# Performance work log

Measured on AMD Instinct MI355X. Metric: run time of the kernel, lower is better.

The kernel has to match this reference:

```python
import jax, jax.numpy as jnp
import numpy as np
from jax import lax

T, B, IN, H, OUT = 2048, 128, 2, 200, 1


def setup_inputs() -> dict:
    key = jax.random.key(0)
    ks = jax.random.split(key, 7)
    s_ih = 1.0 / np.sqrt(H)
    return {
        "input_seq": jax.random.normal(ks[0], (T, B, IN), dtype=jnp.float32),
        "W_ih": jax.random.normal(ks[1], (H, IN), dtype=jnp.float32) * s_ih,
        "W_hh": jax.random.normal(ks[2], (H, H), dtype=jnp.float32) * s_ih,
        "b_ih": jax.random.normal(ks[3], (H,), dtype=jnp.float32) * s_ih,
        "b_hh": jax.random.normal(ks[4], (H,), dtype=jnp.float32) * s_ih,
        "W_out": jax.random.normal(ks[5], (OUT, H), dtype=jnp.float32) * s_ih,
        "b_out": jax.random.normal(ks[6], (OUT,), dtype=jnp.float32) * s_ih,
    }


def reference(input_seq, W_ih, W_hh, b_ih, b_hh, W_out, b_out):
    # torch.nn.RNN (tanh, 1 layer, seq-first): h_t = tanh(x_t W_ih^T + b_ih + h_{t-1} W_hh^T + b_hh)
    # Precompute the input projection for all timesteps (vectorized), fold both biases.
    x_proj = jnp.einsum('tbi,hi->tbh', input_seq, W_ih) + (b_ih + b_hh)  # [T,B,H]

    def step(h, xt):
        h_new = jnp.tanh(xt + h @ W_hh.T)
        return h_new, h_new

    h0 = jnp.zeros((input_seq.shape[1], W_hh.shape[0]), dtype=input_seq.dtype)
    _, hs = lax.scan(step, h0, x_proj)  # hs: [T,B,H]
    # Final linear head applied to every timestep output
    return jnp.einsum('tbh,oh->tbo', hs, W_out) + b_out  # [T,B,1]
```

## Files before the change

kernel.cpp:

```cpp
#include <hip/hip_runtime.h>
#include <hip/hip_fp16.h>


typedef short s8v __attribute__((ext_vector_type(8)));
typedef float f4v __attribute__((ext_vector_type(4)));

static constexpr int T = 2048;
static constexpr int B = 128;
static constexpr int H = 200;
static constexpr int NTHR = 1024;
static constexpr int NT  = 13;
static constexpr int KT  = 7;
static constexpr int HP  = 224;
static constexpr int RS  = 9;

__device__ __forceinline__ unsigned short f2h(float f) {
    const __half h = __float2half_rn(f);
    return *(const unsigned short*)&h;
}
__device__ __forceinline__ float h2f(unsigned short u) {
    const __half h = *(const __half*)&u;
    return __half2float(h);
}

__global__ __attribute__((amdgpu_flat_work_group_size(NTHR, NTHR),
                          amdgpu_waves_per_eu(4, 4)))
void rnn_fused(const float* __restrict__ x,
               const float* __restrict__ W_ih,
               const float* __restrict__ W_hh,
               const float* __restrict__ b_ih,
               const float* __restrict__ b_hh,
               const float* __restrict__ W_out,
               const float* __restrict__ b_out,
               float* __restrict__ out)
{
    const int b    = blockIdx.x;
    const int tid  = threadIdx.x;
    const int w    = tid >> 6;
    const int lane = tid & 63;
    const int m    = lane & 15;
    const int q    = lane >> 4;

    const bool hasT = (w < NT);
    const int  nA   = 16 * w + m;
    const bool colv = hasT && (nA < H);

    __shared__ __align__(16) unsigned short ring[RS][2][HP];
    __shared__ float xs[2 * T];

    for (int i = tid; i < RS * 2 * HP; i += NTHR) (&ring[0][0][0])[i] = 0;
    for (int idx = tid; idx < T; idx += NTHR) {
        const float2 v = *(const float2*)(x + (size_t)idx * (B * 2) + 2 * b);
        xs[2 * idx] = v.x; xs[2 * idx + 1] = v.y;
    }

    s8v BA[KT];
#pragma unroll
    for (int kt = 0; kt < KT; ++kt) {
        s8v ba{};
        if (colv) {
#pragma unroll
            for (int j = 0; j < 8; ++j) {
                const int ks = 32 * kt + 8 * q + j;
                ba[j] = (short)((ks < H) ? f2h(W_hh[nA * H + ks])
                                         : (unsigned short)0);
            }
        }
        BA[kt] = ba;
    }

    const float wxA0 = colv ? W_ih[nA * 2]     : 0.f;
    const float wxA1 = colv ? W_ih[nA * 2 + 1] : 0.f;
    const float bA   = colv ? (b_ih[nA] + b_hh[nA]) : 0.f;

    const float wo0 = W_out[lane];
    const float wo1 = W_out[64 + lane];
    const float wo2 = W_out[128 + lane];
    const float wo3 = (192 + lane < H) ? W_out[192 + lane] : 0.f;
    const float bo  = b_out[0];

    __syncthreads();

    float* op = out + b;

    auto drain = [&](int slot, int tout) {
        float v = (h2f(ring[slot][0][lane])     + h2f(ring[slot][1][lane]))     * wo0
                + (h2f(ring[slot][0][64+lane])  + h2f(ring[slot][1][64+lane]))  * wo1
                + (h2f(ring[slot][0][128+lane]) + h2f(ring[slot][1][128+lane])) * wo2;
        if (lane < 32)
            v += (h2f(ring[slot][0][192+lane]) + h2f(ring[slot][1][192+lane])) * wo3;
#pragma unroll
        for (int off = 32; off > 0; off >>= 1)
            v += __shfl_down(v, off, 64);
        if (lane == 0) op[(size_t)tout * B] = v + bo;
    };

    int rp = 0;
    for (int t = 0; t < T; ++t) {
        if (rp == 0 && t) {
            if (w < RS) drain(w, t - RS + w);
            __syncthreads();
        }
        const int sr = rp ? rp - 1 : RS - 1;
        const int sw = rp;
        const float x0 = xs[2 * t], x1 = xs[2 * t + 1];

        if (hasT) {
            const unsigned short* lp = &ring[sr][(m == 1) ? 1 : 0][8 * q];
            s8v A[KT];
#pragma unroll
            for (int kt = 0; kt < KT; ++kt) A[kt] = *(const s8v*)(lp + 32 * kt);

            f4v u = {0.f, 0.f, 0.f, 0.f};
            f4v v = {0.f, 0.f, 0.f, 0.f};
            u = __builtin_amdgcn_mfma_f32_16x16x32_f16(A[0], BA[0], u, 0, 0, 0);
            v = __builtin_amdgcn_mfma_f32_16x16x32_f16(A[4], BA[4], v, 0, 0, 0);
            u = __builtin_amdgcn_mfma_f32_16x16x32_f16(A[1], BA[1], u, 0, 0, 0);
            v = __builtin_amdgcn_mfma_f32_16x16x32_f16(A[5], BA[5], v, 0, 0, 0);
            u = __builtin_amdgcn_mfma_f32_16x16x32_f16(A[2], BA[2], u, 0, 0, 0);
            v = __builtin_amdgcn_mfma_f32_16x16x32_f16(A[6], BA[6], v, 0, 0, 0);
            u = __builtin_amdgcn_mfma_f32_16x16x32_f16(A[3], BA[3], u, 0, 0, 0);

            if (q == 0 && nA < H) {
                const float y   = (u[0] + u[1]) + (v[0] + v[1]);
                const float pre = y + fmaf(x0, wxA0, fmaf(x1, wxA1, bA));
                const float e   = __expf(2.f * pre);
                const float th  = 1.f - 2.f / (e + 1.f);
                const unsigned short hi = f2h(th);
                ring[sw][0][nA] = hi;
                ring[sw][1][nA] = f2h(th - h2f(hi));
            }
        }
        __syncthreads();
        if (++rp == RS) rp = 0;
    }

    const int rem = T % RS;
    if (w < rem) drain(w, T - rem + w);
}

extern "C" void kernel_launch(void* const* d_in, const int* in_sizes, int n_in,
                              void* d_out, int out_size, void* d_ws, size_t ws_size,
                              hipStream_t stream) {
    const float* x     = (const float*)d_in[0];
    const float* W_ih  = (const float*)d_in[1];
    const float* W_hh  = (const float*)d_in[2];
    const float* b_ih  = (const float*)d_in[3];
    const float* b_hh  = (const float*)d_in[4];
    const float* W_out = (const float*)d_in[5];
    const float* b_out = (const float*)d_in[6];
    float* out = (float*)d_out;

    rnn_fused<<<B, NTHR, 0, stream>>>(x, W_ih, W_hh, b_ih, b_hh, W_out, b_out, out);
}
```

Baseline: 1.114 ms.

## Halve block to 8 waves, each computing two hidden-column tiles per step

Moves the block from 16 waves to 8 and reassigns the 13 hidden-column tiles so most waves compute two tiles, sharing the A fragments loaded from shared memory. The ring buffer shrinks to 8 slots so each wave drains one slot, and the tail drain is simplified because T is divisible by 8. The aim is to make the per-timestep barrier cheaper across fewer waves and to reuse LDS reads, at the cost of longer per-wave MFMA chains and more registers holding the weights.

```diff
diff --git a/kernel.cpp b/kernel.cpp
--- a/kernel.cpp
+++ b/kernel.cpp
@@ -8,11 +8,10 @@
 static constexpr int T = 2048;
 static constexpr int B = 128;
 static constexpr int H = 200;
-static constexpr int NTHR = 1024;
-static constexpr int NT  = 13;
+static constexpr int NTHR = 512;
 static constexpr int KT  = 7;
 static constexpr int HP  = 224;
-static constexpr int RS  = 9;
+static constexpr int RS  = 8;
 
 __device__ __forceinline__ unsigned short f2h(float f) {
     const __half h = __float2half_rn(f);
@@ -24,7 +23,7 @@
 }
 
 __global__ __attribute__((amdgpu_flat_work_group_size(NTHR, NTHR),
-                          amdgpu_waves_per_eu(4, 4)))
+                          amdgpu_waves_per_eu(2, 2)))
 void rnn_fused(const float* __restrict__ x,
                const float* __restrict__ W_ih,
                const float* __restrict__ W_hh,
@@ -41,9 +40,13 @@
     const int m    = lane & 15;
     const int q    = lane >> 4;
 
-    const bool hasT = (w < NT);
-    const int  nA   = 16 * w + m;
-    const bool colv = hasT && (nA < H);
+    const int dfc = (w > 3) + (w > 5) + (w > 6);
+    const int t0  = 2 * w - dfc;
+    const int tn  = (w == 3 || w == 5 || w == 6) ? 1 : 2;
+    const int nA0 = 16 * t0 + m;
+    const int nA1 = 16 * (t0 + 1) + m;
+    const bool cv0 = (nA0 < H);
+    const bool cv1 = (tn > 1) && (nA1 < H);
 
     __shared__ __align__(16) unsigned short ring[RS][2][HP];
     __shared__ float xs[2 * T];
@@ -54,24 +57,35 @@
         xs[2 * idx] = v.x; xs[2 * idx + 1] = v.y;
     }
 
-    s8v BA[KT];
+    s8v BA0[KT], BA1[KT];
 #pragma unroll
     for (int kt = 0; kt < KT; ++kt) {
-        s8v ba{};
-        if (colv) {
+        s8v b0{}, b1{};
+        if (cv0) {
 #pragma unroll
             for (int j = 0; j < 8; ++j) {
                 const int ks = 32 * kt + 8 * q + j;
-                ba[j] = (short)((ks < H) ? f2h(W_hh[nA * H + ks])
+                b0[j] = (short)((ks < H) ? f2h(W_hh[nA0 * H + ks])
                                          : (unsigned short)0);
             }
         }
-        BA[kt] = ba;
+        if (cv1) {
+#pragma unroll
+            for (int j = 0; j < 8; ++j) {
+                const int ks = 32 * kt + 8 * q + j;
+                b1[j] = (short)((ks < H) ? f2h(W_hh[nA1 * H + ks])
+                                         : (unsigned short)0);
+            }
+        }
+        BA0[kt] = b0; BA1[kt] = b1;
     }
 
-    const float wxA0 = colv ? W_ih[nA * 2]     : 0.f;
-    const float wxA1 = colv ? W_ih[nA * 2 + 1] : 0.f;
-    const float bA   = colv ? (b_ih[nA] + b_hh[nA]) : 0.f;
+    const float wx00 = cv0 ? W_ih[nA0 * 2]     : 0.f;
+    const float wx01 = cv0 ? W_ih[nA0 * 2 + 1] : 0.f;
+    const float bA0  = cv0 ? (b_ih[nA0] + b_hh[nA0]) : 0.f;
+    const float wx10 = cv1 ? W_ih[nA1 * 2]     : 0.f;
+    const float wx11 = cv1 ? W_ih[nA1 * 2 + 1] : 0.f;
+    const float bA1  = cv1 ? (b_ih[nA1] + b_hh[nA1]) : 0.f;
 
     const float wo0 = W_out[lane];
     const float wo1 = W_out[64 + lane];
@@ -98,45 +112,84 @@
     int rp = 0;
     for (int t = 0; t < T; ++t) {
         if (rp == 0 && t) {
-            if (w < RS) drain(w, t - RS + w);
+            drain(w, t - RS + w);
             __syncthreads();
         }
         const int sr = rp ? rp - 1 : RS - 1;
         const int sw = rp;
         const float x0 = xs[2 * t], x1 = xs[2 * t + 1];
 
-        if (hasT) {
-            const unsigned short* lp = &ring[sr][(m == 1) ? 1 : 0][8 * q];
-            s8v A[KT];
-#pragma unroll
-            for (int kt = 0; kt < KT; ++kt) A[kt] = *(const s8v*)(lp + 32 * kt);
-
+        const unsigned short* lp = &ring[sr][(m == 1) ? 1 : 0][8 * q];
+        s8v A[KT];
+#pragma unroll
+        for (int kt = 0; kt < KT; ++kt) A[kt] = *(const s8v*)(lp + 32 * kt);
+
+        if (tn == 2) {
+            f4v u0 = {0.f, 0.f, 0.f, 0.f};
+            f4v v0 = {0.f, 0.f, 0.f, 0.f};
+            f4v u1 = {0.f, 0.f, 0.f, 0.f};
+            f4v v1 = {0.f, 0.f, 0.f, 0.f};
+            u0 = __builtin_amdgcn_mfma_f32_16x16x32_f16(A[0], BA0[0], u0, 0, 0, 0);
+            u1 = __builtin_amdgcn_mfma_f32_16x16x32_f16(A[0], BA1[0], u1, 0, 0, 0);
+            v0 = __builtin_amdgcn_mfma_f32_16x16x32_f16(A[4], BA0[4], v0, 0, 0, 0);
+            v1 = __builtin_amdgcn_mfma_f32_16x16x32_f16(A[4], BA1[4], v1, 0, 0, 0);
+            u0 = __builtin_amdgcn_mfma_f32_16x16x32_f16(A[1], BA0[1], u0, 0, 0, 0);
+            u1 = __builtin_amdgcn_mfma_f32_16x16x32_f16(A[1], BA1[1], u1, 0, 0, 0);
+            v0 = __builtin_amdgcn_mfma_f32_16x16x32_f16(A[5], BA0[5], v0, 0, 0, 0);
+            v1 = __builtin_amdgcn_mfma_f32_16x16x32_f16(A[5], BA1[5], v1, 0, 0, 0);
+            u0 = __builtin_amdgcn_mfma_f32_16x16x32_f16(A[2], BA0[2], u0, 0, 0, 0);
+            u1 = __builtin_amdgcn_mfma_f32_16x16x32_f16(A[2], BA1[2], u1, 0, 0, 0);
+            v0 = __builtin_amdgcn_mfma_f32_16x16x32_f16(A[6], BA0[6], v0, 0, 0, 0);
+            v1 = __builtin_amdgcn_mfma_f32_16x16x32_f16(A[6], BA1[6], v1, 0, 0, 0);
+            u0 = __builtin_amdgcn_mfma_f32_16x16x32_f16(A[3], BA0[3], u0, 0, 0, 0);
+            u1 = __builtin_amdgcn_mfma_f32_16x16x32_f16(A[3], BA1[3], u1, 0, 0, 0);
+
+            if (q == 0) {
+                if (cv0) {
+                    const float y   = (u0[0] + u0[1]) + (v0[0] + v0[1]);
+                    const float pre = y + fmaf(x0, wx00, fmaf(x1, wx01, bA0));
+                    const float e   = __expf(2.f * pre);
+                    const float th  = 1.f - 2.f / (e + 1.f);
+                    const unsigned short hi = f2h(th);
+                    ring[sw][0][nA0] = hi;
+                    ring[sw][1][nA0] = f2h(th - h2f(hi));
+                }
+                if (cv1) {
+                    const float y   = (u1[0] + u1[1]) + (v1[0] + v1[1]);
+                    const float pre = y + fmaf(x0, wx10, fmaf(x1, wx11, bA1));
+                    const float e   = __expf(2.f * pre);
+                    const float th  = 1.f - 2.f / (e + 1.f);
+                    const unsigned short hi = f2h(th);
+                    ring[sw][0][nA1] = hi;
+                    ring[sw][1][nA1] = f2h(th - h2f(hi));
+                }
+            }
+        } else {
             f4v u = {0.f, 0.f, 0.f, 0.f};
             f4v v = {0.f, 0.f, 0.f, 0.f};
-            u = __builtin_amdgcn_mfma_f32_16x16x32_f16(A[0], BA[0], u, 0, 0, 0);
-            v = __builtin_amdgcn_mfma_f32_16x16x32_f16(A[4], BA[4], v, 0, 0, 0);
-            u = __builtin_amdgcn_mfma_f32_16x16x32_f16(A[1], BA[1], u, 0, 0, 0);
-            v = __builtin_amdgcn_mfma_f32_16x16x32_f16(A[5], BA[5], v, 0, 0, 0);
-            u = __builtin_amdgcn_mfma_f32_16x16x32_f16(A[2], BA[2], u, 0, 0, 0);
-            v = __builtin_amdgcn_mfma_f32_16x16x32_f16(A[6], BA[6], v, 0, 0, 0);
-            u = __builtin_amdgcn_mfma_f32_16x16x32_f16(A[3], BA[3], u, 0, 0, 0);
-
-            if (q == 0 && nA < H) {
+            u = __builtin_amdgcn_mfma_f32_16x16x32_f16(A[0], BA0[0], u, 0, 0, 0);
+            v = __builtin_amdgcn_mfma_f32_16x16x32_f16(A[4], BA0[4], v, 0, 0, 0);
+            u = __builtin_amdgcn_mfma_f32_16x16x32_f16(A[1], BA0[1], u, 0, 0, 0);
+            v = __builtin_amdgcn_mfma_f32_16x16x32_f16(A[5], BA0[5], v, 0, 0, 0);
+            u = __builtin_amdgcn_mfma_f32_16x16x32_f16(A[2], BA0[2], u, 0, 0, 0);
+            v = __builtin_amdgcn_mfma_f32_16x16x32_f16(A[6], BA0[6], v, 0, 0, 0);
+            u = __builtin_amdgcn_mfma_f32_16x16x32_f16(A[3], BA0[3], u, 0, 0, 0);
+
+            if (q == 0 && cv0) {
                 const float y   = (u[0] + u[1]) + (v[0] + v[1]);
-                const float pre = y + fmaf(x0, wxA0, fmaf(x1, wxA1, bA));
+                const float pre = y + fmaf(x0, wx00, fmaf(x1, wx01, bA0));
                 const float e   = __expf(2.f * pre);
                 const float th  = 1.f - 2.f / (e + 1.f);
                 const unsigned short hi = f2h(th);
-                ring[sw][0][nA] = hi;
-                ring[sw][1][nA] = f2h(th - h2f(hi));
+                ring[sw][0][nA0] = hi;
+                ring[sw][1][nA0] = f2h(th - h2f(hi));
             }
         }
         __syncthreads();
         if (++rp == RS) rp = 0;
     }
 
-    const int rem = T % RS;
-    if (w < rem) drain(w, T - rem + w);
+    drain(w, T - RS + w);
 }
 
 extern "C" void kernel_launch(void* const* d_in, const int* in_sizes, int n_in,
```

Measured after the change: 1.292 ms. 16.0% more time.

## Overlap output-head drain with recurrence using idle waves and batched stores

Applied to the files above, without the earlier changes.

Changes the ring to 8 slots and fully unrolls the time loop in groups of 8. The output-head reduction (drain) now runs on the otherwise idle waves 13 and 14, interleaved with each step instead of stalling every 9th step with an extra barrier. Results are buffered in shared memory and written to global in 64-element batches by wave 15. It also vectorizes the x and W_out loads and splits the MFMA chain into four independent accumulators to shorten the dependency chain. The cost is more complex indexing and an extra shared buffer, with possible hazards around buffer reuse timing.

```diff
diff --git a/kernel.cpp b/kernel.cpp
--- a/kernel.cpp
+++ b/kernel.cpp
@@ -3,6 +3,7 @@
 
 
 typedef short s8v __attribute__((ext_vector_type(8)));
+typedef short s4v __attribute__((ext_vector_type(4)));
 typedef float f4v __attribute__((ext_vector_type(4)));
 
 static constexpr int T = 2048;
@@ -12,7 +13,7 @@
 static constexpr int NT  = 13;
 static constexpr int KT  = 7;
 static constexpr int HP  = 224;
-static constexpr int RS  = 9;
+static constexpr int RS  = 8;
 
 __device__ __forceinline__ unsigned short f2h(float f) {
     const __half h = __float2half_rn(f);
@@ -46,7 +47,8 @@
     const bool colv = hasT && (nA < H);
 
     __shared__ __align__(16) unsigned short ring[RS][2][HP];
-    __shared__ float xs[2 * T];
+    __shared__ __align__(16) float xs[2 * T];
+    __shared__ __align__(16) float obuf[128];
 
     for (int i = tid; i < RS * 2 * HP; i += NTHR) (&ring[0][0][0])[i] = 0;
     for (int idx = tid; idx < T; idx += NTHR) {
@@ -73,70 +75,107 @@
     const float wxA1 = colv ? W_ih[nA * 2 + 1] : 0.f;
     const float bA   = colv ? (b_ih[nA] + b_hh[nA]) : 0.f;
 
-    const float wo0 = W_out[lane];
-    const float wo1 = W_out[64 + lane];
-    const float wo2 = W_out[128 + lane];
-    const float wo3 = (192 + lane < H) ? W_out[192 + lane] : 0.f;
-    const float bo  = b_out[0];
+    const int c4 = 4 * lane;
+    f4v wo = {0.f, 0.f, 0.f, 0.f};
+    if (c4 + 3 < H) wo = *(const f4v*)(W_out + c4);
+    const float bo = b_out[0];
 
     __syncthreads();
 
-    float* op = out + b;
+    const unsigned short* aptr = &ring[0][(m == 1) ? 1 : 0][8 * q];
+    float* const op = out + b;
 
     auto drain = [&](int slot, int tout) {
-        float v = (h2f(ring[slot][0][lane])     + h2f(ring[slot][1][lane]))     * wo0
-                + (h2f(ring[slot][0][64+lane])  + h2f(ring[slot][1][64+lane]))  * wo1
-                + (h2f(ring[slot][0][128+lane]) + h2f(ring[slot][1][128+lane])) * wo2;
-        if (lane < 32)
-            v += (h2f(ring[slot][0][192+lane]) + h2f(ring[slot][1][192+lane])) * wo3;
+        float v = 0.f;
+        if (lane < 56) {
+            const s4v hv = *(const s4v*)(&ring[slot][0][0] + c4);
+            const s4v lv = *(const s4v*)(&ring[slot][1][0] + c4);
+            v = (h2f((unsigned short)hv[0]) + h2f((unsigned short)lv[0])) * wo[0]
+              + (h2f((unsigned short)hv[1]) + h2f((unsigned short)lv[1])) * wo[1]
+              + (h2f((unsigned short)hv[2]) + h2f((unsigned short)lv[2])) * wo[2]
+              + (h2f((unsigned short)hv[3]) + h2f((unsigned short)lv[3])) * wo[3];
+        }
 #pragma unroll
         for (int off = 32; off > 0; off >>= 1)
             v += __shfl_down(v, off, 64);
-        if (lane == 0) op[(size_t)tout * B] = v + bo;
+        if (lane == 0) obuf[tout & 127] = v + bo;
     };
 
-    int rp = 0;
-    for (int t = 0; t < T; ++t) {
-        if (rp == 0 && t) {
-            if (w < RS) drain(w, t - RS + w);
+    for (int t8 = 0; t8 < T / RS; ++t8) {
+        f4v xv0 = {0.f, 0.f, 0.f, 0.f};
+        f4v xv1 = {0.f, 0.f, 0.f, 0.f};
+#pragma unroll
+        for (int rp = 0; rp < RS; ++rp) {
+            const int sr = (rp + RS - 1) & (RS - 1);
+            if (hasT) {
+                if (rp == 0) {
+                    xv0 = *(const f4v*)(xs + 16 * t8);
+                    xv1 = *(const f4v*)(xs + 16 * t8 + 4);
+                } else if (rp == 4) {
+                    xv0 = *(const f4v*)(xs + 16 * t8 + 8);
+                    xv1 = *(const f4v*)(xs + 16 * t8 + 12);
+                }
+                const int r2 = rp & 3;
+                const float x0 = (r2 == 0) ? xv0[0] : (r2 == 1) ? xv0[2]
+                               : (r2 == 2) ? xv1[0] : xv1[2];
+                const float x1 = (r2 == 0) ? xv0[1] : (r2 == 1) ? xv0[3]
+                               : (r2 == 2) ? xv1[1] : xv1[3];
+                const float xterm = fmaf(x0, wxA0, fmaf(x1, wxA1, bA));
+
+                const s8v A0 = *(const s8v*)(aptr + sr * 448 +   0);
+                const s8v A1 = *(const s8v*)(aptr + sr * 448 +  32);
+                const s8v A2 = *(const s8v*)(aptr + sr * 448 +  64);
+                const s8v A3 = *(const s8v*)(aptr + sr * 448 +  96);
+                const s8v A4 = *(const s8v*)(aptr + sr * 448 + 128);
+                const s8v A5 = *(const s8v*)(aptr + sr * 448 + 160);
+                const s8v A6 = *(const s8v*)(aptr + sr * 448 + 192);
+
+                f4v u0 = {0.f, 0.f, 0.f, 0.f};
+                f4v u1 = {0.f, 0.f, 0.f, 0.f};
+                f4v u2 = {0.f, 0.f, 0.f, 0.f};
+                f4v u3 = {0.f, 0.f, 0.f, 0.f};
+                u0 = __builtin_amdgcn_mfma_f32_16x16x32_f16(A0, BA[0], u0, 0, 0, 0);
+                u1 = __builtin_amdgcn_mfma_f32_16x16x32_f16(A2, BA[2], u1, 0, 0, 0);
+                u2 = __builtin_amdgcn_mfma_f32_16x16x32_f16(A4, BA[4], u2, 0, 0, 0);
+                u3 = __builtin_amdgcn_mfma_f32_16x16x32_f16(A6, BA[6], u3, 0, 0, 0);
+                u0 = __builtin_amdgcn_mfma_f32_16x16x32_f16(A1, BA[1], u0, 0, 0, 0);
+                u1 = __builtin_amdgcn_mfma_f32_16x16x32_f16(A3, BA[3], u1, 0, 0, 0);
+                u2 = __builtin_amdgcn_mfma_f32_16x16x32_f16(A5, BA[5], u2, 0, 0, 0);
+
+                if (q == 0 && nA < H) {
+                    const float y = ((u0[0] + u0[1]) + (u1[0] + u1[1]))
+                                  + ((u2[0] + u2[1]) + (u3[0] + u3[1]));
+                    const float pre = y + xterm;
+                    const float e   = __expf(2.f * pre);
+                    const float th  = 1.f - 2.f / (e + 1.f);
+                    const unsigned short hi = f2h(th);
+                    (&ring[rp][0][0])[nA] = hi;
+                    (&ring[rp][1][0])[nA] = f2h(th - h2f(hi));
+                }
+            } else if (w == 13 || w == 14) {
+                if (((rp ^ (w - 13)) & 1) == 0) {
+                    if (rp == 7 || t8 > 0) {
+                        const int t = 8 * t8 + rp;
+                        drain((rp + 1) & 7, t - 7);
+                    }
+                }
+            } else {
+                if (rp == 0 && (t8 & 7) == 1 && t8 > 8) {
+                    const int c = (t8 >> 3) - 1;
+                    const float val = obuf[((c & 1) << 6) | lane];
+                    op[(size_t)(64 * c + lane) * B] = val;
+                }
+            }
             __syncthreads();
         }
-        const int sr = rp ? rp - 1 : RS - 1;
-        const int sw = rp;
-        const float x0 = xs[2 * t], x1 = xs[2 * t + 1];
-
-        if (hasT) {
-            const unsigned short* lp = &ring[sr][(m == 1) ? 1 : 0][8 * q];
-            s8v A[KT];
-#pragma unroll
-            for (int kt = 0; kt < KT; ++kt) A[kt] = *(const s8v*)(lp + 32 * kt);
-
-            f4v u = {0.f, 0.f, 0.f, 0.f};
-            f4v v = {0.f, 0.f, 0.f, 0.f};
-            u = __builtin_amdgcn_mfma_f32_16x16x32_f16(A[0], BA[0], u, 0, 0, 0);
-            v = __builtin_amdgcn_mfma_f32_16x16x32_f16(A[4], BA[4], v, 0, 0, 0);
-            u = __builtin_amdgcn_mfma_f32_16x16x32_f16(A[1], BA[1], u, 0, 0, 0);
-            v = __builtin_amdgcn_mfma_f32_16x16x32_f16(A[5], BA[5], v, 0, 0, 0);
-            u = __builtin_amdgcn_mfma_f32_16x16x32_f16(A[2], BA[2], u, 0, 0, 0);
-            v = __builtin_amdgcn_mfma_f32_16x16x32_f16(A[6], BA[6], v, 0, 0, 0);
-            u = __builtin_amdgcn_mfma_f32_16x16x32_f16(A[3], BA[3], u, 0, 0, 0);
-
-            if (q == 0 && nA < H) {
-                const float y   = (u[0] + u[1]) + (v[0] + v[1]);
-                const float pre = y + fmaf(x0, wxA0, fmaf(x1, wxA1, bA));
-                const float e   = __expf(2.f * pre);
-                const float th  = 1.f - 2.f / (e + 1.f);
-                const unsigned short hi = f2h(th);
-                ring[sw][0][nA] = hi;
-                ring[sw][1][nA] = f2h(th - h2f(hi));
-            }
-        }
-        __syncthreads();
-        if (++rp == RS) rp = 0;
     }
 
-    const int rem = T % RS;
-    if (w < rem) drain(w, T - rem + w);
+    if (w < 7) drain(w + 1, T - 7 + w);
+    __syncthreads();
+    if (w == 15) {
+        const float val = obuf[64 | lane];
+        op[(size_t)(1984 + lane) * B] = val;
+    }
 }
 
 extern "C" void kernel_launch(void* const* d_in, const int* in_sizes, int n_in,
```

Result: slower. 1.292 ms (+16.1%).
